# Performance work log

Measured on AMD Instinct MI355X. Metric: run time of the kernel, lower is better.

## Reference

```python
import jax, jax.numpy as jnp
import numpy as np

N_HEAD = 16

def setup_inputs() -> dict:
    key = jax.random.key(0)
    k0, k1, k2, k3, k4 = jax.random.split(key, 5)
    B, T, C = 4, 2048, 1024
    x = jax.random.normal(k0, (B, T, C), dtype=jnp.float32)
    # torch nn.Linear weights are (out_features, in_features); scale like kaiming-uniform-ish
    s = 1.0 / np.sqrt(C)
    Wk = jax.random.uniform(k1, (C, C), jnp.float32, -s, s)
    Wq = jax.random.uniform(k2, (C, C), jnp.float32, -s, s)
    Wv = jax.random.uniform(k3, (C, C), jnp.float32, -s, s)
    Wo = jax.random.uniform(k4, (C, C), jnp.float32, -s, s)
    return {"x": x, "Wk": Wk, "Wq": Wq, "Wv": Wv, "Wo": Wo}

def reference(x, Wk, Wq, Wv, Wo):
    B, T, C = x.shape
    hs = C // N_HEAD
    # projections (torch Linear: y = x @ W.T), split heads -> (B, nh, T, hs)
    def proj(W):
        return (x @ W.T).reshape(B, T, N_HEAD, hs).transpose(0, 2, 1, 3)
    k = proj(Wk)
    q = proj(Wq)
    v = proj(Wv)
    # dot attention: scale by sqrt(head_dim) (k.shape[2] after transpose in source)
    score = jnp.einsum('bhqd,bhkd->bhqk', q, k) / jnp.sqrt(jnp.asarray(hs, x.dtype))
    # NOTE: source calls score.masked_fill(mask, -inf) without assignment -> mask has no effect.
    e = jax.nn.softmax(score, axis=-1)
    o = jnp.einsum('bhqk,bhkd->bhqd', e, v)          # (B, nh, T, hs)
    o = o.transpose(0, 2, 1, 3).reshape(B, T, C)     # merge heads
    o = o @ Wo.T                                      # final projection
    # dropout is identity in eval mode
    return o
```

## Files before the change

### kernel.cpp

```cpp
#include <hip/hip_runtime.h>
#include <hip/hip_bf16.h>
#include <cstddef>
#include <cstdint>

#define B_DIM 4
#define T_DIM 2048
#define C_DIM 1024
#define NHEAD 16
#define HS    64
#define QKV_LD 3072

#define QSCALE 0.18033688011112042f

typedef __attribute__((ext_vector_type(8))) short short8;
typedef __attribute__((ext_vector_type(4))) float f32x4;

__device__ __forceinline__ short f2bf(float x) {
    __hip_bfloat16 b = __float2bfloat16(x);
    return *reinterpret_cast<short*>(&b);
}

__device__ __forceinline__ void load_lds16(const void* g, void* l) {
    __builtin_amdgcn_global_load_lds(
        (const __attribute__((address_space(1))) void*)(g),
        (__attribute__((address_space(3))) void*)(l),
        16, 0, 0);
}

__global__ __launch_bounds__(256) void cast_bf16(
    const float* __restrict__ in, short* __restrict__ out, int n8, float scale)
{
    int i = blockIdx.x * 256 + threadIdx.x;
    if (i >= n8) return;
    const float4* p = (const float4*)in + (size_t)i * 2;
    float4 a = p[0], b = p[1];
    short8 o;
    o[0]=f2bf(a.x*scale); o[1]=f2bf(a.y*scale); o[2]=f2bf(a.z*scale); o[3]=f2bf(a.w*scale);
    o[4]=f2bf(b.x*scale); o[5]=f2bf(b.y*scale); o[6]=f2bf(b.z*scale); o[7]=f2bf(b.w*scale);
    *((short8*)out + i) = o;
}

__global__ __launch_bounds__(256) void cast4_bf16(
    const float* __restrict__ w0, const float* __restrict__ w1,
    const float* __restrict__ w2, const float* __restrict__ w3,
    short* __restrict__ out, int n8)
{
    int i = blockIdx.x * 256 + threadIdx.x;
    if (i >= n8) return;
    const int sel = blockIdx.y;
    const float* in = (sel == 0) ? w0 : (sel == 1) ? w1 : (sel == 2) ? w2 : w3;
    const float scale = (sel == 0) ? QSCALE : 1.0f;
    const float4* p = (const float4*)in + (size_t)i * 2;
    float4 a = p[0], b = p[1];
    short8 o;
    o[0]=f2bf(a.x*scale); o[1]=f2bf(a.y*scale); o[2]=f2bf(a.z*scale); o[3]=f2bf(a.w*scale);
    o[4]=f2bf(b.x*scale); o[5]=f2bf(b.y*scale); o[6]=f2bf(b.z*scale); o[7]=f2bf(b.w*scale);
    *((short8*)out + (size_t)sel * n8 + i) = o;
}

template<bool OUT_BF16>
__global__ __launch_bounds__(512, 2) void gemm_bt_8ph(
    const short* __restrict__ A,
    const short* __restrict__ Bm,
    void* __restrict__ Cm,
    int M, int N, int K)
{
    __shared__ __align__(16) short lds[49152];

    const int nbx = N >> 8;
    int wg = blockIdx.x;
    const int cpx = gridDim.x >> 3;
    wg = (wg & 7) * cpx + (wg >> 3);
    const int bx = wg % nbx, by = wg / nbx;
    const int m0 = by << 7, n0 = bx << 8;

    const int t = threadIdx.x;
    const int w = t >> 6, lane = t & 63;
    const int l16 = lane & 15, quad = lane >> 4;
    const int wm = w >> 2, wn = w & 3;

    const int rcall  = t >> 3;
    const int schunk = (t & 7) ^ (rcall & 7);
    const int dstoff = w * 512;

    const short* Ag = A  + (size_t)(m0 + rcall) * K + schunk * 8;
    const short* Bg = Bm + (size_t)(n0 + rcall) * K + schunk * 8;

    short* const Ab0 = lds;
    short* const Ab1 = lds + 8192;
    short* const Bb0 = lds + 16384;
    short* const Bb1 = lds + 32768;

    int aoff[4][2], boff[4][2];
    #pragma unroll
    for (int mf = 0; mf < 4; ++mf) {
        const int ar = wm * 64 + mf * 16 + l16;
        #pragma unroll
        for (int ks = 0; ks < 2; ++ks)
            aoff[mf][ks] = ar * 64 + (((ks * 4 + quad) ^ (ar & 7)) * 8);
    }
    #pragma unroll
    for (int nf = 0; nf < 4; ++nf) {
        const int br = wn * 64 + nf * 16 + l16;
        #pragma unroll
        for (int ks = 0; ks < 2; ++ks)
            boff[nf][ks] = br * 64 + (((ks * 4 + quad) ^ (br & 7)) * 8);
    }

    f32x4 acc[4][4];
    const f32x4 zero4 = {0.f, 0.f, 0.f, 0.f};
    #pragma unroll
    for (int mf = 0; mf < 4; ++mf)
        #pragma unroll
        for (int nf = 0; nf < 4; ++nf) acc[mf][nf] = zero4;

    const int NT = K >> 6;

    #define ST64(gb, kt, ro, lb)                                               \
        load_lds16((gb) + (size_t)(ro) * K + (size_t)(kt) * 64,                \
                   (lb) + (ro) * 64 + dstoff)

    ST64(Ag, 0, 0, Ab0); ST64(Ag, 0, 64, Ab0);
    ST64(Bg, 0, 0, Bb0); ST64(Bg, 0, 64, Bb0);
    ST64(Bg, 0, 128, Bb0); ST64(Bg, 0, 192, Bb0);
    ST64(Ag, 1, 0, Ab1); ST64(Ag, 1, 64, Ab1);

    for (int kt = 0; kt < NT; ++kt) {
        short* Acur = (kt & 1) ? Ab1 : Ab0;
        short* Bcur = (kt & 1) ? Bb1 : Bb0;
        short* Bnx  = (kt & 1) ? Bb0 : Bb1;

        if (kt == NT - 1) asm volatile("s_waitcnt vmcnt(0)" ::: "memory");
        else              asm volatile("s_waitcnt vmcnt(2)" ::: "memory");
        __builtin_amdgcn_s_barrier();

        short8 bfr[4][2], af[2][2];
        #pragma unroll
        for (int nf = 0; nf < 4; ++nf)
            #pragma unroll
            for (int ks = 0; ks < 2; ++ks)
                bfr[nf][ks] = *(const short8*)(Bcur + boff[nf][ks]);
        #pragma unroll
        for (int mf = 0; mf < 2; ++mf)
            #pragma unroll
            for (int ks = 0; ks < 2; ++ks)
                af[mf][ks] = *(const short8*)(Acur + aoff[mf][ks]);

        if (kt + 1 < NT) { ST64(Bg, kt + 1, 0, Bnx); ST64(Bg, kt + 1, 64, Bnx); }

        __builtin_amdgcn_s_barrier();
        __builtin_amdgcn_s_setprio(1);
        #pragma unroll
        for (int mf = 0; mf < 2; ++mf)
            #pragma unroll
            for (int nf = 0; nf < 4; ++nf)
                #pragma unroll
                for (int ks = 0; ks < 2; ++ks)
                    acc[mf][nf] = __builtin_amdgcn_mfma_f32_16x16x32_bf16(
                        af[mf][ks], bfr[nf][ks], acc[mf][nf], 0, 0, 0);
        __builtin_amdgcn_s_setprio(0);
        __builtin_amdgcn_s_barrier();

        short8 af2[2][2];
        #pragma unroll
        for (int mf = 0; mf < 2; ++mf)
            #pragma unroll
            for (int ks = 0; ks < 2; ++ks)
                af2[mf][ks] = *(const short8*)(Acur + aoff[2 + mf][ks]);

        if (kt + 1 < NT) { ST64(Bg, kt + 1, 128, Bnx); ST64(Bg, kt + 1, 192, Bnx); }

        __builtin_amdgcn_s_barrier();
        __builtin_amdgcn_s_setprio(1);
        #pragma unroll
        for (int mf = 0; mf < 2; ++mf)
            #pragma unroll
            for (int nf = 0; nf < 4; ++nf)
                #pragma unroll
                for (int ks = 0; ks < 2; ++ks)
                    acc[2 + mf][nf] = __builtin_amdgcn_mfma_f32_16x16x32_bf16(
                        af2[mf][ks], bfr[nf][ks], acc[2 + mf][nf], 0, 0, 0);
        __builtin_amdgcn_s_setprio(0);
        __builtin_amdgcn_s_barrier();

        if (kt + 2 < NT) {
            short* Aw = (kt & 1) ? Ab1 : Ab0;
            ST64(Ag, kt + 2, 0, Aw); ST64(Ag, kt + 2, 64, Aw);
        }
    }
    #undef ST64

    #pragma unroll
    for (int mf = 0; mf < 4; ++mf) {
        const int row_base = m0 + wm * 64 + mf * 16 + quad * 4;
        #pragma unroll
        for (int nf = 0; nf < 4; ++nf) {
            const int col = n0 + wn * 64 + nf * 16 + l16;
            #pragma unroll
            for (int r = 0; r < 4; ++r) {
                const size_t idx = (size_t)(row_base + r) * N + col;
                if (OUT_BF16) ((short*)Cm)[idx] = f2bf(acc[mf][nf][r]);
                else          ((float*)Cm)[idx] = acc[mf][nf][r];
            }
        }
    }
}

__global__ __launch_bounds__(256) void transpose_v(
    const short* __restrict__ Vb,
    short* __restrict__ Vt, int srcLD)
{
    const int t0 = blockIdx.x * 64;
    const int head = blockIdx.y;
    const int b = head >> 4, h = head & 15;

    __shared__ short Ls[64][72];

    const int t = threadIdx.x;
    const int r = t >> 2;
    const int c = (t & 3) * 16;

    const short* src = Vb + ((size_t)(b * T_DIM) + t0 + r) * srcLD + h * HS + c;
    *(short8*)&Ls[r][c]     = *(const short8*)src;
    *(short8*)&Ls[r][c + 8] = *(const short8*)(src + 8);
    __syncthreads();

    short tmp[16];
    #pragma unroll
    for (int i = 0; i < 16; ++i) tmp[i] = Ls[c + i][r];
    short* dst = Vt + ((size_t)head * HS + r) * T_DIM + t0 + c;
    *(short8*)dst       = *(short8*)&tmp[0];
    *(short8*)(dst + 8) = *(short8*)&tmp[8];
}

#define QSUB 2

__global__ __launch_bounds__(256, 4) void attn_mfma3(
    const short* __restrict__ Qb,
    const short* __restrict__ Kb,
    const short* __restrict__ Vt,
    short* __restrict__ O)
{
    const int i0   = blockIdx.x * (64 * QSUB);
    const int head = blockIdx.y;
    const int b = head >> 4, h = head & 15;

    const int t    = threadIdx.x;
    const int w    = t >> 6;
    const int lane = t & 63;
    const int l16  = lane & 15;
    const int quad = lane >> 4;

    __shared__ short Ks[64][72];
    __shared__ short Vts[64][72];

    short8 qf[QSUB][2];
    #pragma unroll
    for (int sub = 0; sub < QSUB; ++sub) {
        const short* qrow = Qb
            + ((size_t)(b * T_DIM) + i0 + sub * 64 + w * 16 + l16) * QKV_LD + h * HS;
        qf[sub][0] = *(const short8*)(qrow + quad * 8);
        qf[sub][1] = *(const short8*)(qrow + 32 + quad * 8);
    }

    short8 onesv;
    #pragma unroll
    for (int j = 0; j < 8; ++j) onesv[j] = (short)0x3F80;

    const f32x4 zero4 = {0.f, 0.f, 0.f, 0.f};
    f32x4 oacc[QSUB][4];
    f32x4 lacc[QSUB];
    #pragma unroll
    for (int sub = 0; sub < QSUB; ++sub) {
        #pragma unroll
        for (int dg = 0; dg < 4; ++dg) oacc[sub][dg] = zero4;
        lacc[sub] = zero4;
    }

    const int sr = t >> 2;
    const int sc = (t & 3) * 16;
    const int krow = (sr & 32) | ((sr & 4) << 2) | ((sr & 24) >> 1) | (sr & 3);
    const short* kgbase = Kb + (size_t)(b * T_DIM) * QKV_LD + h * HS;
    const short* vgbase = Vt + ((size_t)head * HS + sr) * T_DIM;

    for (int j0 = 0; j0 < T_DIM; j0 += 64) {
        __syncthreads();
        {
            const short* kp = kgbase + (size_t)(j0 + sr) * QKV_LD + sc;
            *(short8*)&Ks[krow][sc]     = *(const short8*)kp;
            *(short8*)&Ks[krow][sc + 8] = *(const short8*)(kp + 8);
            const short* vp = vgbase + j0 + sc;
            *(short8*)&Vts[sr][sc]      = *(const short8*)vp;
            *(short8*)&Vts[sr][sc + 8]  = *(const short8*)(vp + 8);
        }
        __syncthreads();

        short8 ka[4][2], va[4][2];
        #pragma unroll
        for (int kt = 0; kt < 4; ++kt) {
            ka[kt][0] = *(const short8*)&Ks[kt * 16 + l16][quad * 8];
            ka[kt][1] = *(const short8*)&Ks[kt * 16 + l16][32 + quad * 8];
            va[kt][0] = *(const short8*)&Vts[kt * 16 + l16][quad * 8];
            va[kt][1] = *(const short8*)&Vts[kt * 16 + l16][32 + quad * 8];
        }

        #pragma unroll
        for (int sub = 0; sub < QSUB; ++sub) {
            f32x4 s[4];
            #pragma unroll
            for (int kt = 0; kt < 4; ++kt) {
                f32x4 acc = zero4;
                acc = __builtin_amdgcn_mfma_f32_16x16x32_bf16(ka[kt][0], qf[sub][0], acc, 0, 0, 0);
                acc = __builtin_amdgcn_mfma_f32_16x16x32_bf16(ka[kt][1], qf[sub][1], acc, 0, 0, 0);
                s[kt] = acc;
            }

            short8 pa[2];
            #pragma unroll
            for (int hh = 0; hh < 2; ++hh) {
                #pragma unroll
                for (int c = 0; c < 2; ++c) {
                    f32x4 sv = s[2 * hh + c];
                    #pragma unroll
                    for (int r = 0; r < 4; ++r) {
                        float p = __builtin_amdgcn_exp2f(sv[r]);
                        pa[hh][c * 4 + r] = f2bf(p);
                    }
                }
            }

            lacc[sub] = __builtin_amdgcn_mfma_f32_16x16x32_bf16(pa[0], onesv, lacc[sub], 0, 0, 0);
            lacc[sub] = __builtin_amdgcn_mfma_f32_16x16x32_bf16(pa[1], onesv, lacc[sub], 0, 0, 0);

            #pragma unroll
            for (int dg = 0; dg < 4; ++dg) {
                oacc[sub][dg] = __builtin_amdgcn_mfma_f32_16x16x32_bf16(pa[0], va[dg][0], oacc[sub][dg], 0, 0, 0);
                oacc[sub][dg] = __builtin_amdgcn_mfma_f32_16x16x32_bf16(pa[1], va[dg][1], oacc[sub][dg], 0, 0, 0);
            }
        }
    }

    #pragma unroll
    for (int sub = 0; sub < QSUB; ++sub) {
        float linv[4];
        #pragma unroll
        for (int r = 0; r < 4; ++r) linv[r] = 1.0f / lacc[sub][r];

        #pragma unroll
        for (int r = 0; r < 4; ++r) {
            short* orow = O + ((size_t)(b * T_DIM) + i0 + sub * 64 + w * 16 + quad * 4 + r) * C_DIM + h * HS;
            #pragma unroll
            for (int dg = 0; dg < 4; ++dg)
                orow[dg * 16 + l16] = f2bf(oacc[sub][dg][r] * linv[r]);
        }
    }
}

extern "C" void kernel_launch(void* const* d_in, const int* in_sizes, int n_in,
                              void* d_out, int out_size, void* d_ws, size_t ws_size,
                              hipStream_t stream) {
    const float* x  = (const float*)d_in[0];
    const float* Wk = (const float*)d_in[1];
    const float* Wq = (const float*)d_in[2];
    const float* Wv = (const float*)d_in[3];
    const float* Wo = (const float*)d_in[4];
    float* out = (float*)d_out;

    const int M = B_DIM * T_DIM;
    const size_t NE = (size_t)M * C_DIM;
    const size_t NB = 2 * NE;
    const size_t WB = (size_t)2 * C_DIM * C_DIM;
    const size_t WE = (size_t)C_DIM * C_DIM;

    char* ws = (char*)d_ws;
    short* xb   = (short*)(ws);
    short* Ob   = xb;
    short* QKVb = (short*)(ws + NB);
    short* Vtb  = (short*)(ws + 4 * NB);
    short* W3b  = (short*)(ws + 5 * NB);
    short* Wob  = (short*)(ws + 5 * NB + 3 * WB);

    cast_bf16<<<(int)(NE / 8 / 256), 256, 0, stream>>>(x, xb, (int)(NE / 8), 1.0f);
    const int wn8 = (int)(WE / 8);
    cast4_bf16<<<dim3(wn8 / 256, 4), 256, 0, stream>>>(Wq, Wk, Wv, Wo, W3b, wn8);

    gemm_bt_8ph<true><<<dim3((QKV_LD / 256) * (M / 128)), 512, 0, stream>>>(
        xb, W3b, QKVb, M, QKV_LD, C_DIM);

    transpose_v<<<dim3(T_DIM / 64, B_DIM * NHEAD), 256, 0, stream>>>(
        QKVb + 2 * C_DIM, Vtb, QKV_LD);

    attn_mfma3<<<dim3(T_DIM / (64 * QSUB), B_DIM * NHEAD), 256, 0, stream>>>(
        QKVb, QKVb + C_DIM, Vtb, Ob);

    gemm_bt_8ph<false><<<dim3((C_DIM / 256) * (M / 128)), 512, 0, stream>>>(
        Ob, Wob, out, M, C_DIM, C_DIM);
}
```

Before: 259.6 us.

## Fuse V transpose into QKV GEMM epilogue and remap attention grid per XCD

The QKV GEMM epilogue now writes the V portion directly in transposed per-head layout, which removes the separate transpose kernel and its extra pass over V. The attention kernel is launched on a 1D grid whose block index is remapped so that blocks of the same head land on the same XCD, meant to improve L2 reuse of K/V. The transposed epilogue stores are strided short4 writes, which are less coalesced than the row-major stores.

```diff
diff --git a/kernel.cpp b/kernel.cpp
--- a/kernel.cpp
+++ b/kernel.cpp
@@ -13,6 +13,7 @@
 #define QSCALE 0.18033688011112042f
 
 typedef __attribute__((ext_vector_type(8))) short short8;
+typedef __attribute__((ext_vector_type(4))) short short4v;
 typedef __attribute__((ext_vector_type(4))) float f32x4;
 
 __device__ __forceinline__ short f2bf(float x) {
@@ -58,11 +59,12 @@
     *((short8*)out + (size_t)sel * n8 + i) = o;
 }
 
-template<bool OUT_BF16>
+template<int OUT_MODE>
 __global__ __launch_bounds__(512, 2) void gemm_bt_8ph(
     const short* __restrict__ A,
     const short* __restrict__ Bm,
     void* __restrict__ Cm,
+    short* __restrict__ Vt,
     int M, int N, int K)
 {
     __shared__ __align__(16) short lds[49152];
@@ -190,47 +192,40 @@
     }
     #undef ST64
 
-    #pragma unroll
-    for (int mf = 0; mf < 4; ++mf) {
-        const int row_base = m0 + wm * 64 + mf * 16 + quad * 4;
+    if (OUT_MODE == 2 && n0 >= 2 * C_DIM) {
+        const int b    = m0 >> 11;
+        const int tt0  = (m0 & 2047) + wm * 64 + quad * 4;
         #pragma unroll
         for (int nf = 0; nf < 4; ++nf) {
-            const int col = n0 + wn * 64 + nf * 16 + l16;
-            #pragma unroll
-            for (int r = 0; r < 4; ++r) {
-                const size_t idx = (size_t)(row_base + r) * N + col;
-                if (OUT_BF16) ((short*)Cm)[idx] = f2bf(acc[mf][nf][r]);
-                else          ((float*)Cm)[idx] = acc[mf][nf][r];
-            }
-        }
-    }
-}
-
-__global__ __launch_bounds__(256) void transpose_v(
-    const short* __restrict__ Vb,
-    short* __restrict__ Vt, int srcLD)
-{
-    const int t0 = blockIdx.x * 64;
-    const int head = blockIdx.y;
-    const int b = head >> 4, h = head & 15;
-
-    __shared__ short Ls[64][72];
-
-    const int t = threadIdx.x;
-    const int r = t >> 2;
-    const int c = (t & 3) * 16;
-
-    const short* src = Vb + ((size_t)(b * T_DIM) + t0 + r) * srcLD + h * HS + c;
-    *(short8*)&Ls[r][c]     = *(const short8*)src;
-    *(short8*)&Ls[r][c + 8] = *(const short8*)(src + 8);
-    __syncthreads();
-
-    short tmp[16];
-    #pragma unroll
-    for (int i = 0; i < 16; ++i) tmp[i] = Ls[c + i][r];
-    short* dst = Vt + ((size_t)head * HS + r) * T_DIM + t0 + c;
-    *(short8*)dst       = *(short8*)&tmp[0];
-    *(short8*)(dst + 8) = *(short8*)&tmp[8];
+            const int vcol = (n0 - 2 * C_DIM) + wn * 64 + nf * 16 + l16;
+            const int h    = vcol >> 6;
+            const int d    = vcol & 63;
+            short* dcol = Vt + ((size_t)((b << 4) + h) * HS + d) * T_DIM;
+            #pragma unroll
+            for (int mf = 0; mf < 4; ++mf) {
+                const int tt = tt0 + mf * 16;
+                short4v o;
+                o[0] = f2bf(acc[mf][nf][0]); o[1] = f2bf(acc[mf][nf][1]);
+                o[2] = f2bf(acc[mf][nf][2]); o[3] = f2bf(acc[mf][nf][3]);
+                *(short4v*)(dcol + tt) = o;
+            }
+        }
+    } else {
+        #pragma unroll
+        for (int mf = 0; mf < 4; ++mf) {
+            const int row_base = m0 + wm * 64 + mf * 16 + quad * 4;
+            #pragma unroll
+            for (int nf = 0; nf < 4; ++nf) {
+                const int col = n0 + wn * 64 + nf * 16 + l16;
+                #pragma unroll
+                for (int r = 0; r < 4; ++r) {
+                    const size_t idx = (size_t)(row_base + r) * N + col;
+                    if (OUT_MODE != 0) ((short*)Cm)[idx] = f2bf(acc[mf][nf][r]);
+                    else               ((float*)Cm)[idx] = acc[mf][nf][r];
+                }
+            }
+        }
+    }
 }
 
 #define QSUB 2
@@ -241,8 +236,10 @@
     const short* __restrict__ Vt,
     short* __restrict__ O)
 {
-    const int i0   = blockIdx.x * (64 * QSUB);
-    const int head = blockIdx.y;
+    const int bid  = blockIdx.x;
+    const int slot = bid >> 3;
+    const int head = ((bid & 7) << 3) + (slot >> 4);
+    const int i0   = (slot & 15) * (64 * QSUB);
     const int b = head >> 4, h = head & 15;
 
     const int t    = threadIdx.x;
@@ -384,15 +381,12 @@
     const int wn8 = (int)(WE / 8);
     cast4_bf16<<<dim3(wn8 / 256, 4), 256, 0, stream>>>(Wq, Wk, Wv, Wo, W3b, wn8);
 
-    gemm_bt_8ph<true><<<dim3((QKV_LD / 256) * (M / 128)), 512, 0, stream>>>(
-        xb, W3b, QKVb, M, QKV_LD, C_DIM);
-
-    transpose_v<<<dim3(T_DIM / 64, B_DIM * NHEAD), 256, 0, stream>>>(
-        QKVb + 2 * C_DIM, Vtb, QKV_LD);
-
-    attn_mfma3<<<dim3(T_DIM / (64 * QSUB), B_DIM * NHEAD), 256, 0, stream>>>(
+    gemm_bt_8ph<2><<<dim3((QKV_LD / 256) * (M / 128)), 512, 0, stream>>>(
+        xb, W3b, QKVb, Vtb, M, QKV_LD, C_DIM);
+
+    attn_mfma3<<<dim3(T_DIM / (64 * QSUB) * B_DIM * NHEAD), 256, 0, stream>>>(
         QKVb, QKVb + C_DIM, Vtb, Ob);
 
-    gemm_bt_8ph<false><<<dim3((C_DIM / 256) * (M / 128)), 512, 0, stream>>>(
-        Ob, Wob, out, M, C_DIM, C_DIM);
-}
+    gemm_bt_8ph<0><<<dim3((C_DIM / 256) * (M / 128)), 512, 0, stream>>>(
+        Ob, Wob, out, nullptr, M, C_DIM, C_DIM);
+}
```

New measurement: 254.6 us. Within noise of the previous version (-1.9%).
